# Kernel optimization log

Hardware: AMD Instinct MI355X
Metric: run time of the kernel (lower is better)

Reference implementation:

```python
import jax, jax.numpy as jnp
import numpy as np

B, N, D = 128, 512, 128      # graphs, nodes/graph, feature dim
KEEP_RATIO = 0.5
K = int(KEEP_RATIO * N)      # kept nodes per graph (fixed -> jit friendly)
EDGE_P = 0.05                # random graph edge density


def setup_inputs() -> dict:
    key = jax.random.key(0)
    k1, k2, k3 = jax.random.split(key, 3)
    # random symmetric binary adjacency without self loops, per graph block
    u = jax.random.uniform(k1, (B, N, N))
    a0 = (u < EDGE_P).astype(jnp.float32)
    a0 = jnp.maximum(a0, jnp.swapaxes(a0, 1, 2))
    eye = jnp.eye(N, dtype=jnp.float32)
    a0 = a0 * (1.0 - eye)
    # normalized input adjacency: D^-0.5 (A0 + I) D^-0.5 (as `normalization` does)
    a_hat = a0 + eye
    dinv = a_hat.sum(-1) ** -0.5
    adjacency = a_hat * dinv[:, :, None] * dinv[:, None, :]   # [B,N,N]
    input_feature = jax.random.normal(k2, (B, N, D), dtype=jnp.float32)
    graph_indicator = jnp.repeat(jnp.arange(B, dtype=jnp.int32), N)  # [B*N]
    # attn_gcn params: Linear(D -> 1) kaiming-style init, zero bias
    weight = jax.random.normal(k3, (D, 1), dtype=jnp.float32) * (2.0 / D) ** 0.5
    bias = jnp.zeros((1,), dtype=jnp.float32)
    return {"adjacency": adjacency, "input_feature": input_feature,
            "graph_indicator": graph_indicator, "weight": weight, "bias": bias}


def reference(adjacency, input_feature, graph_indicator, weight, bias):
    # --- attention GCN: Z = A @ (X W) + b, then tanh ---
    support = jnp.einsum('bnd,do->bno', input_feature, weight)      # [B,N,1]
    score = jnp.einsum('bnm,bmo->bno', adjacency, support) + bias   # [B,N,1]
    attn = jnp.tanh(score[..., 0])                                  # [B,N]
    # --- top_rank: per-graph top-K by score; mask preserves node order ---
    _, idx = jax.lax.top_k(attn, K)                                 # [B,K]
    idx = jnp.sort(idx, axis=-1)                                    # original node order
    # --- hidden = X[mask] * attn[mask] ---
    kept_x = jnp.take_along_axis(input_feature, idx[:, :, None], axis=1)  # [B,K,D]
    kept_s = jnp.take_along_axis(attn, idx, axis=1)                       # [B,K]
    hidden = (kept_x * kept_s[:, :, None]).reshape(B * K, D)
    mask_graph_indicator = jnp.repeat(jnp.arange(B, dtype=graph_indicator.dtype), K)
    # --- filter_adjacency: binarize off-diagonal structure, gather, renormalize ---
    eye_n = jnp.eye(N, dtype=adjacency.dtype)
    a_bin = jnp.where((adjacency != 0) & (eye_n == 0), 1.0, 0.0)    # [B,N,N]
    rows = jnp.take_along_axis(a_bin, idx[:, :, None], axis=1)      # [B,K,N]
    sub = jnp.take_along_axis(rows, idx[:, None, :], axis=2)        # [B,K,K]
    a_hat = sub + jnp.eye(K, dtype=adjacency.dtype)
    dinv = a_hat.sum(-1) ** -0.5
    mask_adjacency = a_hat * dinv[:, :, None] * dinv[:, None, :]    # [B,K,K]
    return hidden, mask_graph_indicator, mask_adjacency
```

## Files before the change

### kernel.cpp

```cpp
#include <hip/hip_runtime.h>
#include <hip/hip_bf16.h>
#include <math.h>

#define BGR 128
#define NND 512
#define DFD 128
#define KKP 256

typedef unsigned int uint;
typedef unsigned long long ull;

__global__ __launch_bounds__(256) void k_support(const float* __restrict__ X,
                                                 const float* __restrict__ W,
                                                 float* __restrict__ sup) {
    __shared__ float w_s[DFD];
    int t = threadIdx.x;
    if (t < DFD) w_s[t] = W[t];
    __syncthreads();
    int node = blockIdx.x * 64 + (t >> 2);
    int q = t & 3;
    const float4* xp = (const float4*)(X + (size_t)node * DFD + q * 32);
    const float4* wp = (const float4*)(w_s + q * 32);
    float sum = 0.f;
#pragma unroll
    for (int i = 0; i < 8; ++i) {
        float4 x = xp[i], w = wp[i];
        sum += x.x * w.x + x.y * w.y + x.z * w.z + x.w * w.w;
    }
    sum += __shfl_xor(sum, 1);
    sum += __shfl_xor(sum, 2);
    if (q == 0) sup[node] = sum;
}

__global__ __launch_bounds__(256) void k_score(const float* __restrict__ A,
                                               const float* __restrict__ sup,
                                               const float* __restrict__ bias,
                                               float* __restrict__ attn,
                                               ull* __restrict__ bm) {
    __shared__ float sup_s[NND];
    int b = blockIdx.x >> 6;
    int rblk = blockIdx.x & 63;
    int t = threadIdx.x;
    sup_s[t] = sup[b * NND + t];
    sup_s[256 + t] = sup[b * NND + 256 + t];
    __syncthreads();
    int wave = t >> 6, l = t & 63;
    float bias0 = bias[0];
    const float4* sp = (const float4*)sup_s;
    float4 s0 = sp[l], s1 = sp[64 + l];
#pragma unroll
    for (int r = 0; r < 2; ++r) {
        int row = rblk * 8 + wave * 2 + r;
        const float4* ap = (const float4*)(A + ((size_t)b * NND + row) * NND);
        float4 a0 = ap[l], a1 = ap[64 + l];
        float sum = a0.x * s0.x + a0.y * s0.y + a0.z * s0.z + a0.w * s0.w
                  + a1.x * s1.x + a1.y * s1.y + a1.z * s1.z + a1.w * s1.w;
        int c0 = 4 * l;
        ull m[8];
        m[0] = __ballot(a0.x != 0.f && (c0 + 0) != row);
        m[1] = __ballot(a0.y != 0.f && (c0 + 1) != row);
        m[2] = __ballot(a0.z != 0.f && (c0 + 2) != row);
        m[3] = __ballot(a0.w != 0.f && (c0 + 3) != row);
        m[4] = __ballot(a1.x != 0.f && (256 + c0 + 0) != row);
        m[5] = __ballot(a1.y != 0.f && (256 + c0 + 1) != row);
        m[6] = __ballot(a1.z != 0.f && (256 + c0 + 2) != row);
        m[7] = __ballot(a1.w != 0.f && (256 + c0 + 3) != row);
#pragma unroll
        for (int off = 32; off >= 1; off >>= 1) sum += __shfl_down(sum, off);
        if (l == 0) {
            attn[b * NND + row] = tanhf(sum + bias0);
            ull* bp = bm + ((size_t)b * NND + row) * 8;
#pragma unroll
            for (int k = 0; k < 8; ++k) bp[k] = m[k];
        }
    }
}

__global__ __launch_bounds__(512) void k_mega(const float* __restrict__ X,
                                              const float* __restrict__ attn,
                                              const uint* __restrict__ bm,
                                              float* __restrict__ out_hidden,
                                              float* __restrict__ out_gi,
                                              float* __restrict__ out_adj) {
    __shared__ float attn_s[NND];
    __shared__ uint km[16];
    __shared__ int idx_s[KKP];
    __shared__ uint4 bm_s4[KKP][4];
    __shared__ uint bits_s[KKP][8];
    __shared__ float dinv_s[KKP];
    int b = blockIdx.x >> 2, q = blockIdx.x & 3;
    int t = threadIdx.x, wave = t >> 6, l = t & 63;
    attn_s[t] = attn[b * NND + t];
    __syncthreads();

    float a = attn_s[t];
    int r = 0;
    const float4* ap4 = (const float4*)attn_s;
    for (int jj = 0; jj < 128; ++jj) {
        float4 v = ap4[jj];
        int j0 = jj * 4;
        r += (v.x > a || (v.x == a && j0     < t)) ? 1 : 0;
        r += (v.y > a || (v.y == a && j0 + 1 < t)) ? 1 : 0;
        r += (v.z > a || (v.z == a && j0 + 2 < t)) ? 1 : 0;
        r += (v.w > a || (v.w == a && j0 + 3 < t)) ? 1 : 0;
    }
    bool keep = r < KKP;
    ull mk = __ballot(keep);
    if (l == 0) { km[wave * 2] = (uint)mk; km[wave * 2 + 1] = (uint)(mk >> 32); }
    __syncthreads();
    if (keep) {
        int w = t >> 5, pos = 0;
        for (int u = 0; u < w; ++u) pos += __popc(km[u]);
        pos += __popc(km[w] & ((1u << (t & 31)) - 1u));
        idx_s[pos] = t;
    }
    __syncthreads();

    {
        int i = t >> 1, half = t & 1;
        const uint4* src = (const uint4*)(bm + ((size_t)b * NND + idx_s[i]) * 16) + half * 2;
        bm_s4[i][half * 2]     = src[0];
        bm_s4[i][half * 2 + 1] = src[1];
    }

    if (t < KKP) out_gi[b * KKP + t] = (float)b;
#pragma unroll
    for (int it = 0; it < 8; ++it) {
        int k = q * 64 + it * 8 + wave;
        int node = idx_s[k];
        float s = attn_s[node];
        const float2* xp = (const float2*)(X + ((size_t)b * NND + node) * DFD);
        float2 v = xp[l];
        v.x *= s; v.y *= s;
        ((float2*)(out_hidden + ((size_t)b * KKP + k) * DFD))[l] = v;
    }
    __syncthreads();

    const uint* bmw = (const uint*)bm_s4;
    int jn = idx_s[t & 255];
    int widx = ((jn >> 8) * 4 + (jn & 3)) * 2 + ((jn >> 7) & 1);
    int bitpos = (jn >> 2) & 31;
    int rowoff = t >> 8;
    int wq = (t >> 6) & 3;
    for (int ii = 0; ii < KKP; ii += 2) {
        int row = ii + rowoff;
        uint kb = (bmw[row * 16 + widx] >> bitpos) & 1u;
        ull mb = __ballot(kb != 0u);
        if (l == 0) {
            bits_s[row][wq * 2]     = (uint)mb;
            bits_s[row][wq * 2 + 1] = (uint)(mb >> 32);
        }
    }
    __syncthreads();
    if (t < KKP) {
        int s = 1;
#pragma unroll
        for (int k = 0; k < 8; ++k) s += __popc(bits_s[t][k]);
        dinv_s[t] = 1.0f / sqrtf((float)s);
    }
    __syncthreads();

    float4 dj = ((const float4*)dinv_s)[l];
    const float* djp = &dj.x;
#pragma unroll
    for (int it = 0; it < 8; ++it) {
        int i = q * 64 + it * 8 + wave;
        float di = dinv_s[i];
        uint word = bits_s[i][l >> 3];
        int j0 = l * 4;
        float4 v;
        float* pv = &v.x;
#pragma unroll
        for (int c = 0; c < 4; ++c) {
            int j = j0 + c;
            float ah = ((word >> (j & 31)) & 1u) ? 1.0f : 0.0f;
            if (j == i) ah += 1.0f;
            pv[c] = ah * di * djp[c];
        }
        ((float4*)(out_adj + ((size_t)b * KKP + i) * KKP))[l] = v;
    }
}

extern "C" void kernel_launch(void* const* d_in, const int* in_sizes, int n_in,
                              void* d_out, int out_size, void* d_ws, size_t ws_size,
                              hipStream_t stream) {
    const float* A    = (const float*)d_in[0];
    const float* X    = (const float*)d_in[1];
    const float* W    = (const float*)d_in[3];
    const float* bias = (const float*)d_in[4];

    float* out        = (float*)d_out;
    float* out_hidden = out;
    float* out_gi     = out + (size_t)BGR * KKP * DFD;
    float* out_adj    = out_gi + (size_t)BGR * KKP;

    float* sup  = (float*)d_ws;
    float* attn = sup + (size_t)BGR * NND;
    ull*   bm   = (ull*)(attn + (size_t)BGR * NND);

    k_support<<<BGR * NND / 64, 256, 0, stream>>>(X, W, sup);
    k_score<<<BGR * 64, 256, 0, stream>>>(A, sup, bias, attn, bm);
    k_mega<<<BGR * 4, 512, 0, stream>>>(X, attn, (const uint*)bm,
                                        out_hidden, out_gi, out_adj);
}
```

Measured before the change: 70.32 us.

## Use nontemporal loads/stores, more rows per score block, split mega kernel wider

The score kernel now processes 32 rows per block (two rows interleaved per iteration, with 2x unroll) using nontemporal loads of the adjacency, and writes the bitmasks as 128-bit vector stores. The mega kernel is split into 8 blocks per graph instead of 4, with nontemporal stores for the hidden and adjacency outputs. The goal is more memory-level parallelism when streaming the 128 MB adjacency and less cache pollution. The cost is that each extra mega block repeats the per-graph rank and bitmask work, and score has fewer blocks in flight.

```diff
diff --git a/kernel.cpp b/kernel.cpp
--- a/kernel.cpp
+++ b/kernel.cpp
@@ -9,6 +9,13 @@
 
 typedef unsigned int uint;
 typedef unsigned long long ull;
+typedef float  fvec4 __attribute__((ext_vector_type(4)));
+typedef float  fvec2 __attribute__((ext_vector_type(2)));
+typedef uint   uvec4 __attribute__((ext_vector_type(4)));
+
+__device__ inline fvec4 ntload4(const float* p) {
+    return __builtin_nontemporal_load((const fvec4*)p);
+}
 
 __global__ __launch_bounds__(256) void k_support(const float* __restrict__ X,
                                                  const float* __restrict__ W,
@@ -38,40 +45,65 @@
                                                float* __restrict__ attn,
                                                ull* __restrict__ bm) {
     __shared__ float sup_s[NND];
-    int b = blockIdx.x >> 6;
-    int rblk = blockIdx.x & 63;
+    int b = blockIdx.x >> 4;
+    int rblk = blockIdx.x & 15;
     int t = threadIdx.x;
-    sup_s[t] = sup[b * NND + t];
-    sup_s[256 + t] = sup[b * NND + 256 + t];
+    if (t < 128) ((float4*)sup_s)[t] = ((const float4*)(sup + (size_t)b * NND))[t];
     __syncthreads();
     int wave = t >> 6, l = t & 63;
     float bias0 = bias[0];
     const float4* sp = (const float4*)sup_s;
     float4 s0 = sp[l], s1 = sp[64 + l];
-#pragma unroll
-    for (int r = 0; r < 2; ++r) {
-        int row = rblk * 8 + wave * 2 + r;
-        const float4* ap = (const float4*)(A + ((size_t)b * NND + row) * NND);
-        float4 a0 = ap[l], a1 = ap[64 + l];
-        float sum = a0.x * s0.x + a0.y * s0.y + a0.z * s0.z + a0.w * s0.w
-                  + a1.x * s1.x + a1.y * s1.y + a1.z * s1.z + a1.w * s1.w;
-        int c0 = 4 * l;
-        ull m[8];
-        m[0] = __ballot(a0.x != 0.f && (c0 + 0) != row);
-        m[1] = __ballot(a0.y != 0.f && (c0 + 1) != row);
-        m[2] = __ballot(a0.z != 0.f && (c0 + 2) != row);
-        m[3] = __ballot(a0.w != 0.f && (c0 + 3) != row);
-        m[4] = __ballot(a1.x != 0.f && (256 + c0 + 0) != row);
-        m[5] = __ballot(a1.y != 0.f && (256 + c0 + 1) != row);
-        m[6] = __ballot(a1.z != 0.f && (256 + c0 + 2) != row);
-        m[7] = __ballot(a1.w != 0.f && (256 + c0 + 3) != row);
-#pragma unroll
-        for (int off = 32; off >= 1; off >>= 1) sum += __shfl_down(sum, off);
+    int c0 = 4 * l;
+    int row0 = rblk * 32 + wave * 8;
+#pragma unroll 2
+    for (int pr = 0; pr < 4; ++pr) {
+        int rowA = row0 + pr * 2;
+        int rowB = rowA + 1;
+        const float* apA = A + ((size_t)b * NND + rowA) * NND;
+        const float* apB = A + ((size_t)b * NND + rowB) * NND;
+        fvec4 a0 = ntload4(apA + 4 * l),   a1 = ntload4(apA + 256 + 4 * l);
+        fvec4 b0 = ntload4(apB + 4 * l),   b1 = ntload4(apB + 256 + 4 * l);
+        float sA = a0.x * s0.x + a0.y * s0.y + a0.z * s0.z + a0.w * s0.w
+                 + a1.x * s1.x + a1.y * s1.y + a1.z * s1.z + a1.w * s1.w;
+        float sB = b0.x * s0.x + b0.y * s0.y + b0.z * s0.z + b0.w * s0.w
+                 + b1.x * s1.x + b1.y * s1.y + b1.z * s1.z + b1.w * s1.w;
+        ull mA[8], mB[8];
+        mA[0] = __ballot(a0.x != 0.f && (c0 + 0) != rowA);
+        mA[1] = __ballot(a0.y != 0.f && (c0 + 1) != rowA);
+        mA[2] = __ballot(a0.z != 0.f && (c0 + 2) != rowA);
+        mA[3] = __ballot(a0.w != 0.f && (c0 + 3) != rowA);
+        mA[4] = __ballot(a1.x != 0.f && (256 + c0 + 0) != rowA);
+        mA[5] = __ballot(a1.y != 0.f && (256 + c0 + 1) != rowA);
+        mA[6] = __ballot(a1.z != 0.f && (256 + c0 + 2) != rowA);
+        mA[7] = __ballot(a1.w != 0.f && (256 + c0 + 3) != rowA);
+        mB[0] = __ballot(b0.x != 0.f && (c0 + 0) != rowB);
+        mB[1] = __ballot(b0.y != 0.f && (c0 + 1) != rowB);
+        mB[2] = __ballot(b0.z != 0.f && (c0 + 2) != rowB);
+        mB[3] = __ballot(b0.w != 0.f && (c0 + 3) != rowB);
+        mB[4] = __ballot(b1.x != 0.f && (256 + c0 + 0) != rowB);
+        mB[5] = __ballot(b1.y != 0.f && (256 + c0 + 1) != rowB);
+        mB[6] = __ballot(b1.z != 0.f && (256 + c0 + 2) != rowB);
+        mB[7] = __ballot(b1.w != 0.f && (256 + c0 + 3) != rowB);
+#pragma unroll
+        for (int off = 32; off >= 1; off >>= 1) {
+            sA += __shfl_xor(sA, off);
+            sB += __shfl_xor(sB, off);
+        }
         if (l == 0) {
-            attn[b * NND + row] = tanhf(sum + bias0);
-            ull* bp = bm + ((size_t)b * NND + row) * 8;
-#pragma unroll
-            for (int k = 0; k < 8; ++k) bp[k] = m[k];
+            attn[b * NND + rowA] = tanhf(sA + bias0);
+            attn[b * NND + rowB] = tanhf(sB + bias0);
+            uint* bpA = (uint*)(bm + ((size_t)b * NND + rowA) * 8);
+            uint* bpB = (uint*)(bm + ((size_t)b * NND + rowB) * 8);
+#pragma unroll
+            for (int k = 0; k < 4; ++k) {
+                uvec4 wA = { (uint)mA[2*k], (uint)(mA[2*k] >> 32),
+                             (uint)mA[2*k+1], (uint)(mA[2*k+1] >> 32) };
+                uvec4 wB = { (uint)mB[2*k], (uint)(mB[2*k] >> 32),
+                             (uint)mB[2*k+1], (uint)(mB[2*k+1] >> 32) };
+                *((uvec4*)bpA + k) = wA;
+                *((uvec4*)bpB + k) = wB;
+            }
         }
     }
 }
@@ -88,7 +120,7 @@
     __shared__ uint4 bm_s4[KKP][4];
     __shared__ uint bits_s[KKP][8];
     __shared__ float dinv_s[KKP];
-    int b = blockIdx.x >> 2, q = blockIdx.x & 3;
+    int b = blockIdx.x >> 3, q = blockIdx.x & 7;
     int t = threadIdx.x, wave = t >> 6, l = t & 63;
     attn_s[t] = attn[b * NND + t];
     __syncthreads();
@@ -123,16 +155,16 @@
         bm_s4[i][half * 2 + 1] = src[1];
     }
 
-    if (t < KKP) out_gi[b * KKP + t] = (float)b;
-#pragma unroll
-    for (int it = 0; it < 8; ++it) {
-        int k = q * 64 + it * 8 + wave;
+    if (q == 0 && t < KKP) out_gi[b * KKP + t] = (float)b;
+#pragma unroll
+    for (int it = 0; it < 4; ++it) {
+        int k = q * 32 + it * 8 + wave;
         int node = idx_s[k];
         float s = attn_s[node];
         const float2* xp = (const float2*)(X + ((size_t)b * NND + node) * DFD);
         float2 v = xp[l];
-        v.x *= s; v.y *= s;
-        ((float2*)(out_hidden + ((size_t)b * KKP + k) * DFD))[l] = v;
+        fvec2 v2 = { v.x * s, v.y * s };
+        __builtin_nontemporal_store(v2, (fvec2*)(out_hidden + ((size_t)b * KKP + k) * DFD) + l);
     }
     __syncthreads();
 
@@ -163,21 +195,20 @@
     float4 dj = ((const float4*)dinv_s)[l];
     const float* djp = &dj.x;
 #pragma unroll
-    for (int it = 0; it < 8; ++it) {
-        int i = q * 64 + it * 8 + wave;
+    for (int it = 0; it < 4; ++it) {
+        int i = q * 32 + it * 8 + wave;
         float di = dinv_s[i];
         uint word = bits_s[i][l >> 3];
         int j0 = l * 4;
-        float4 v;
-        float* pv = &v.x;
+        fvec4 v;
 #pragma unroll
         for (int c = 0; c < 4; ++c) {
             int j = j0 + c;
             float ah = ((word >> (j & 31)) & 1u) ? 1.0f : 0.0f;
             if (j == i) ah += 1.0f;
-            pv[c] = ah * di * djp[c];
-        }
-        ((float4*)(out_adj + ((size_t)b * KKP + i) * KKP))[l] = v;
+            v[c] = ah * di * djp[c];
+        }
+        __builtin_nontemporal_store(v, (fvec4*)(out_adj + ((size_t)b * KKP + i) * KKP) + l);
     }
 }
 
@@ -199,7 +230,7 @@
     ull*   bm   = (ull*)(attn + (size_t)BGR * NND);
 
     k_support<<<BGR * NND / 64, 256, 0, stream>>>(X, W, sup);
-    k_score<<<BGR * 64, 256, 0, stream>>>(A, sup, bias, attn, bm);
-    k_mega<<<BGR * 4, 512, 0, stream>>>(X, attn, (const uint*)bm,
+    k_score<<<BGR * 16, 256, 0, stream>>>(A, sup, bias, attn, bm);
+    k_mega<<<BGR * 8, 512, 0, stream>>>(X, attn, (const uint*)bm,
                                         out_hidden, out_gi, out_adj);
 }
```

New measurement: 86.45 us. 1.23x slower.
